# Kernel tuning notes

Measured on AMD Instinct MI355X. Metric: run time of the kernel, lower is better.

The kernel has to match this reference:

```python
import jax, jax.numpy as jnp
import numpy as np

D_MODEL = 1024
D_FF = 4096
N_EXPERTS = 4
D_HID = D_MODEL // 2
TOP_K = 2
B, T = 2, 4096


def setup_inputs() -> dict:
    key = jax.random.key(0)
    ks = jax.random.split(key, 10)
    s_in = 1.0 / np.sqrt(D_MODEL)
    s_ff = 1.0 / np.sqrt(D_FF)
    s_h = 1.0 / np.sqrt(D_HID)
    return {
        "x": jax.random.normal(ks[0], (B, T, D_MODEL), jnp.float32),
        # stacked expert FFN params [E, ...]
        "w1": jax.random.normal(ks[1], (N_EXPERTS, D_MODEL, D_FF), jnp.float32) * s_in,
        "b1": jnp.zeros((N_EXPERTS, D_FF), jnp.float32),
        "w2": jax.random.normal(ks[2], (N_EXPERTS, D_FF, D_MODEL), jnp.float32) * s_ff,
        "b2": jnp.zeros((N_EXPERTS, D_MODEL), jnp.float32),
        # router MLP params
        "wr1": jax.random.normal(ks[3], (D_MODEL, D_HID), jnp.float32) * s_in,
        "br1": jnp.zeros((D_HID,), jnp.float32),
        "wr2": jax.random.normal(ks[4], (D_HID, N_EXPERTS), jnp.float32) * s_h,
        "br2": jnp.zeros((N_EXPERTS,), jnp.float32),
    }


def _gelu(x):
    return jax.nn.gelu(x, approximate=False)  # torch nn.GELU default is exact erf


def reference(x, w1, b1, w2, b2, wr1, br1, wr2, br2):
    # Router: 2-layer MLP -> logits [B,T,E]
    h = _gelu(jnp.einsum('btd,dh->bth', x, wr1) + br1)
    logits = jnp.einsum('bth,he->bte', h, wr2) + br2
    # top-k masked softmax over experts
    top_vals, _ = jax.lax.top_k(logits, TOP_K)
    thresh = top_vals[..., -1:]
    masked = jnp.where(logits >= thresh, logits, -jnp.inf)
    gate = jax.nn.softmax(masked, axis=-1)  # [B,T,E], zeros off top-k
    # dense all-experts FFN: hid [B,T,E,d_ff]
    hid = _gelu(jnp.einsum('btd,edf->btef', x, w1) + b1)
    expert_outs = jnp.einsum('btef,efd->bted', hid, w2) + b2  # [B,T,E,d_model]
    out = jnp.einsum('bte,bted->btd', gate, expert_outs)
    return out, gate
```

## Files before the change

kernel.cpp:

```cpp
#include <hip/hip_runtime.h>

#define NTOK 8192
#define DM 1024
#define DF 4096
#define DH 512
#define NE 4
#define SLOTS (NTOK * 2)
#define NYT_MAX 132

typedef unsigned short ushort_t;
typedef short bf16x8 __attribute__((ext_vector_type(8)));
typedef float f32x4 __attribute__((ext_vector_type(4)));

__device__ __forceinline__ unsigned short f2bf(float f) {
    unsigned int u = __float_as_uint(f);
    u += 0x7FFFu + ((u >> 16) & 1u);
    return (unsigned short)(u >> 16);
}
__device__ __forceinline__ float bf2f(unsigned short h) {
    return __uint_as_float(((unsigned int)h) << 16);
}
__device__ __forceinline__ float gelu_exact(float x) {
    return 0.5f * x * (1.0f + erff(x * 0.7071067811865476f));
}
__device__ __forceinline__ float gelu_fast(float x) {
    float u = 1.5957691216057308f * (x + 0.044715f * x * x * x);
    return x / (1.0f + __expf(-u));
}
__device__ __forceinline__ void gload16(const void* g, void* l) {
    __builtin_amdgcn_global_load_lds((__attribute__((address_space(1))) void*)(g),
                                     (__attribute__((address_space(3))) void*)(l), 16, 0, 0);
}
__device__ __forceinline__ int swz(int b) { return b ^ (((b >> 7) & 3) << 4); }
__device__ __forceinline__ int imin(int a, int b) { return a < b ? a : b; }

#define WAIT_VM(N) asm volatile("s_waitcnt vmcnt(" #N ")" ::: "memory")
#define WAIT_LGKM0() asm volatile("s_waitcnt lgkmcnt(0)" ::: "memory")
#define SBAR() __builtin_amdgcn_s_barrier()
#define SCHED0() __builtin_amdgcn_sched_barrier(0)

__global__ __launch_bounds__(256) void k_cast_split(const float* __restrict__ in,
                                                    ushort_t* __restrict__ hi,
                                                    ushort_t* __restrict__ lo, int n4) {
    int i = blockIdx.x * 256 + threadIdx.x;
    if (i >= n4) return;
    float4 v = ((const float4*)in)[i];
    ushort4 h, l;
    h.x = f2bf(v.x); l.x = f2bf(v.x - bf2f(h.x));
    h.y = f2bf(v.y); l.y = f2bf(v.y - bf2f(h.y));
    h.z = f2bf(v.z); l.z = f2bf(v.z - bf2f(h.z));
    h.w = f2bf(v.w); l.w = f2bf(v.w - bf2f(h.w));
    ((ushort4*)hi)[i] = h;
    ((ushort4*)lo)[i] = l;
}

template <bool SPLIT>
__global__ __launch_bounds__(256) void k_tcast(const float* __restrict__ in,
                                               ushort_t* __restrict__ oh,
                                               ushort_t* __restrict__ ol, int K, int N) {
    __shared__ float t[64][65];
    size_t base = (size_t)blockIdx.z * K * N;
    const float* src = in + base;
    int k0 = blockIdx.y * 64, n0 = blockIdx.x * 64;
    int tx = threadIdx.x & 63, ty = threadIdx.x >> 6;
#pragma unroll
    for (int i = 0; i < 16; i++) {
        int r = ty + i * 4;
        t[r][tx] = src[(size_t)(k0 + r) * N + n0 + tx];
    }
    __syncthreads();
#pragma unroll
    for (int i = 0; i < 16; i++) {
        int nn = ty + i * 4;
        float v = t[tx][nn];
        unsigned short hv = f2bf(v);
        size_t o = base + (size_t)(n0 + nn) * K + k0 + tx;
        oh[o] = hv;
        if (SPLIT) ol[o] = f2bf(v - bf2f(hv));
    }
}

__global__ __launch_bounds__(256) void k_rgemm(
    const ushort_t* __restrict__ A0, const ushort_t* __restrict__ B0,
    const ushort_t* __restrict__ A1, const ushort_t* __restrict__ B1,
    const ushort_t* __restrict__ A2, const ushort_t* __restrict__ B2,
    int K, int N, const float* __restrict__ bias, float* __restrict__ outF)
{
    __shared__ ushort_t lA[3][4096];
    __shared__ ushort_t lB[3][4096];
    int row0 = blockIdx.y * 128, col0 = blockIdx.x * 128;
    int tid = threadIdx.x, lane = tid & 63, wv = tid >> 6;
    int wr = wv >> 1, wc = wv & 1;
    int r15 = lane & 15, hq = lane >> 4;

    f32x4 z = {0.f, 0.f, 0.f, 0.f};
    f32x4 acc[4][4];
#pragma unroll
    for (int m = 0; m < 4; m++)
#pragma unroll
        for (int n = 0; n < 4; n++) acc[m][n] = z;

    int d0 = tid * 16, d1 = d0 + 4096;
    int u0 = swz(d0), u1 = swz(d1);
    int rA0 = u0 >> 6, ko0 = ((u0 >> 4) & 3) * 8;
    int rA1 = u1 >> 6, ko1 = ((u1 >> 4) & 3) * 8;
    int nstep = K / 32;

#pragma unroll 1
    for (int p = 0; p < 3; p++) {
        const ushort_t* A = (p == 0) ? A0 : ((p == 1) ? A1 : A2);
        const ushort_t* B = (p == 0) ? B0 : ((p == 1) ? B1 : B2);
        const ushort_t* Ab0 = A + (size_t)(row0 + rA0) * K + ko0;
        const ushort_t* Ab1 = A + (size_t)(row0 + rA1) * K + ko1;
        const ushort_t* Bb0 = B + (size_t)(col0 + rA0) * K + ko0;
        const ushort_t* Bb1 = B + (size_t)(col0 + rA1) * K + ko1;

        auto stage = [&](int b, int s) {
            int kt = s * 32;
            char* la = (char*)lA + b * 8192;
            char* lb = (char*)lB + b * 8192;
            gload16(Ab0 + kt, la + wv * 1024);
            gload16(Ab1 + kt, la + 4096 + wv * 1024);
            gload16(Bb0 + kt, lb + wv * 1024);
            gload16(Bb1 + kt, lb + 4096 + wv * 1024);
        };
        auto compute = [&](int b) {
            const char* pa = (const char*)lA + b * 8192;
            const char* pb = (const char*)lB + b * 8192;
            bf16x8 af[4], bfr[4];
#pragma unroll
            for (int m = 0; m < 4; m++)
                af[m] = *(const bf16x8*)(pa + swz(((wr * 64 + m * 16 + r15) << 6) + (hq << 4)));
#pragma unroll
            for (int n = 0; n < 4; n++)
                bfr[n] = *(const bf16x8*)(pb + swz(((wc * 64 + n * 16 + r15) << 6) + (hq << 4)));
            __builtin_amdgcn_s_setprio(1);
#pragma unroll
            for (int m = 0; m < 4; m++)
#pragma unroll
                for (int n = 0; n < 4; n++)
                    acc[m][n] = __builtin_amdgcn_mfma_f32_16x16x32_bf16(af[m], bfr[n], acc[m][n], 0, 0, 0);
            __builtin_amdgcn_s_setprio(0);
        };

        stage(0, 0); stage(1, 1); stage(2, 2);
        int cur = 0;
#pragma unroll 1
        for (int s = 0; s < nstep - 3; s++) {
            WAIT_VM(8); SBAR(); SCHED0();
            compute(cur);
            WAIT_LGKM0(); SCHED0(); SBAR(); SCHED0();
            stage(cur, s + 3);
            cur = (cur == 2) ? 0 : cur + 1;
        }
        WAIT_VM(8); SBAR(); SCHED0();
        compute(cur); cur = (cur == 2) ? 0 : cur + 1;
        WAIT_VM(4); SBAR(); SCHED0();
        compute(cur); cur = (cur == 2) ? 0 : cur + 1;
        WAIT_VM(0); SBAR(); SCHED0();
        compute(cur);
        WAIT_LGKM0(); SCHED0(); SBAR(); SCHED0();
    }

#pragma unroll
    for (int m = 0; m < 4; m++)
#pragma unroll
        for (int q = 0; q < 4; q++) {
            int row = row0 + wr * 64 + m * 16 + hq * 4 + q;
#pragma unroll
            for (int n = 0; n < 4; n++) {
                int col = col0 + wc * 64 + n * 16 + r15;
                outF[(size_t)row * N + col] = gelu_exact(acc[m][n][q] + bias[col]);
            }
        }
}

template <int MODE>
__global__ __launch_bounds__(512, 4) void k_egemm(
    const ushort_t* __restrict__ A0, const ushort_t* __restrict__ B0,
    const float* __restrict__ bias, const float* __restrict__ gate,
    const int* __restrict__ idx, const int4* __restrict__ tiles,
    const int* __restrict__ meta,
    ushort_t* __restrict__ ghid, float* __restrict__ outA)
{
    constexpr int K = (MODE == 1) ? DM : DF;
    constexpr int NFULL = (MODE == 1) ? DF : DM;
    constexpr int NXT = NFULL / 256;
    constexpr int nwg = NXT * NYT_MAX;
    constexpr int q8 = nwg / 8;
    constexpr int NSTEP = K / 32;

    int bid = blockIdx.x;
    int wgid = (bid & 7) * q8 + (bid >> 3);
    int xt = wgid / NYT_MAX, yt = wgid % NYT_MAX;
    if (yt >= meta[0]) return;
    int4 ti = tiles[yt];
    int e = ti.x, rstart = ti.y, rows = ti.z, gbase = ti.w;
    int col0 = xt * 256;

    __shared__ ushort_t lA[3][4096];
    __shared__ ushort_t lB[3][8192];
    int tid = threadIdx.x, lane = tid & 63, wv = tid >> 6;
    int wr = wv >> 2, wc = wv & 3;
    int r15 = lane & 15, hq = lane >> 4;

    f32x4 z = {0.f, 0.f, 0.f, 0.f};
    f32x4 acc[4][4];
#pragma unroll
    for (int m = 0; m < 4; m++)
#pragma unroll
        for (int n = 0; n < 4; n++) acc[m][n] = z;

    int u = swz(tid * 16);
    int rA = u >> 6;
    int ko = ((u >> 4) & 3) * 8;
    const ushort_t *Ab, *Bb0, *Bb1;
    if (MODE == 1) {
        int tok = idx[e * NTOK + rstart + imin(rA, rows - 1)];
        Ab = A0 + (size_t)tok * K + ko;
    } else {
        Ab = A0 + (size_t)(gbase + imin(rA, rows - 1)) * K + ko;
    }
    Bb0 = B0 + ((size_t)e * NFULL + col0 + rA) * K + ko;
    Bb1 = B0 + ((size_t)e * NFULL + col0 + 128 + rA) * K + ko;

    auto stage = [&](int b, int s) {
        int kt = s * 32;
        gload16(Ab + kt, (char*)lA + b * 8192 + wv * 1024);
        gload16(Bb0 + kt, (char*)lB + b * 16384 + wv * 1024);
        gload16(Bb1 + kt, (char*)lB + b * 16384 + 8192 + wv * 1024);
    };
    auto compute = [&](int b) {
        const char* pa = (const char*)lA + b * 8192;
        const char* pb = (const char*)lB + b * 16384;
        bf16x8 af[4], bfr[4];
#pragma unroll
        for (int m = 0; m < 4; m++)
            af[m] = *(const bf16x8*)(pa + swz(((wr * 64 + m * 16 + r15) << 6) + (hq << 4)));
#pragma unroll
        for (int n = 0; n < 4; n++)
            bfr[n] = *(const bf16x8*)(pb + swz(((wc * 64 + n * 16 + r15) << 6) + (hq << 4)));
        __builtin_amdgcn_s_setprio(1);
#pragma unroll
        for (int m = 0; m < 4; m++)
#pragma unroll
            for (int n = 0; n < 4; n++)
                acc[m][n] = __builtin_amdgcn_mfma_f32_16x16x32_bf16(af[m], bfr[n], acc[m][n], 0, 0, 0);
        __builtin_amdgcn_s_setprio(0);
    };

    stage(0, 0); stage(1, 1); stage(2, 2);
    int cur = 0;
#pragma unroll 1
    for (int s = 0; s < NSTEP - 3; s++) {
        WAIT_VM(6); SBAR(); SCHED0();
        compute(cur);
        WAIT_LGKM0(); SCHED0(); SBAR(); SCHED0();
        stage(cur, s + 3);
        cur = (cur == 2) ? 0 : cur + 1;
    }
    WAIT_VM(6); SBAR(); SCHED0();
    compute(cur); cur = (cur == 2) ? 0 : cur + 1;
    WAIT_VM(3); SBAR(); SCHED0();
    compute(cur); cur = (cur == 2) ? 0 : cur + 1;
    WAIT_VM(0); SBAR(); SCHED0();
    compute(cur);

    if (MODE == 1) {
#pragma unroll
        for (int m = 0; m < 4; m++)
#pragma unroll
            for (int q = 0; q < 4; q++) {
                int lr = wr * 64 + m * 16 + hq * 4 + q;
                if (lr < rows) {
                    int token = idx[e * NTOK + rstart + lr];
                    float g = gate[token * 4 + e];
                    size_t rb = (size_t)(gbase + lr) * NFULL;
#pragma unroll
                    for (int n = 0; n < 4; n++) {
                        int col = col0 + wc * 64 + n * 16 + r15;
                        float v = gelu_fast(acc[m][n][q] + bias[(size_t)e * NFULL + col]) * g;
                        ghid[rb + col] = f2bf(v);
                    }
                }
            }
    } else {
#pragma unroll
        for (int m = 0; m < 4; m++)
#pragma unroll
            for (int q = 0; q < 4; q++) {
                int lr = wr * 64 + m * 16 + hq * 4 + q;
                if (lr < rows) {
                    int token = idx[e * NTOK + rstart + lr];
#pragma unroll
                    for (int n = 0; n < 4; n++) {
                        int col = col0 + wc * 64 + n * 16 + r15;
                        atomicAdd(&outA[(size_t)token * NFULL + col], acc[m][n][q]);
                    }
                }
            }
    }
}

__global__ __launch_bounds__(256) void k_gate(const float* __restrict__ h,
                                              const float* __restrict__ wr2,
                                              const float* __restrict__ br2,
                                              float* __restrict__ gate,
                                              int* __restrict__ cnt,
                                              int* __restrict__ idx) {
    int t = blockIdx.x * 4 + (threadIdx.x >> 6);
    int lane = threadIdx.x & 63;
    const float* hr = h + (size_t)t * DH;
    const float4* w4 = (const float4*)wr2;
    float gx = 0.f, gy = 0.f, gz = 0.f, gw = 0.f;
#pragma unroll
    for (int j = 0; j < 8; j++) {
        int k = lane * 8 + j;
        float hv = hr[k];
        float4 w = w4[k];
        gx += hv * w.x; gy += hv * w.y; gz += hv * w.z; gw += hv * w.w;
    }
#pragma unroll
    for (int off = 32; off > 0; off >>= 1) {
        gx += __shfl_xor(gx, off);
        gy += __shfl_xor(gy, off);
        gz += __shfl_xor(gz, off);
        gw += __shfl_xor(gw, off);
    }
    if (lane == 0) {
        float ls[4];
        ls[0] = gx + br2[0]; ls[1] = gy + br2[1]; ls[2] = gz + br2[2]; ls[3] = gw + br2[3];
        int i1 = 0; float m1 = ls[0];
#pragma unroll
        for (int i = 1; i < 4; i++) if (ls[i] > m1) { m1 = ls[i]; i1 = i; }
        int i2 = -1; float m2 = -1e30f;
#pragma unroll
        for (int i = 0; i < 4; i++) if (i != i1 && ls[i] > m2) { m2 = ls[i]; i2 = i; }
        float e0 = (ls[0] >= m2) ? expf(ls[0] - m1) : 0.f;
        float e1 = (ls[1] >= m2) ? expf(ls[1] - m1) : 0.f;
        float e2 = (ls[2] >= m2) ? expf(ls[2] - m1) : 0.f;
        float e3 = (ls[3] >= m2) ? expf(ls[3] - m1) : 0.f;
        float iz = 1.f / (e0 + e1 + e2 + e3);
        float4 g = {e0 * iz, e1 * iz, e2 * iz, e3 * iz};
        ((float4*)gate)[t] = g;
        int s0 = atomicAdd(&cnt[i1], 1);
        idx[i1 * NTOK + s0] = t;
        int s1 = atomicAdd(&cnt[i2], 1);
        idx[i2 * NTOK + s1] = t;
    }
}

__global__ void k_tiles(const int* __restrict__ cnt, int4* __restrict__ tiles,
                        int* __restrict__ meta) {
    if (threadIdx.x != 0 || blockIdx.x != 0) return;
    int base = 0, nt = 0;
    for (int e = 0; e < NE; e++) {
        int c = cnt[e];
        for (int r = 0; r < c; r += 128) {
            int4 ti;
            ti.x = e; ti.y = r; ti.z = (c - r < 128) ? (c - r) : 128; ti.w = base + r;
            tiles[nt++] = ti;
        }
        base += c;
    }
    meta[0] = nt;
}

__global__ __launch_bounds__(256) void k_init_out(const float* __restrict__ gate,
                                                  const float* __restrict__ b2,
                                                  float* __restrict__ out) {
    int i = blockIdx.x * 256 + threadIdx.x;
    int t = i >> 8;
    int c4 = i & 255;
    float4 g = ((const float4*)gate)[t];
    const float4* b = (const float4*)b2;
    float4 v0 = b[c4], v1 = b[256 + c4], v2 = b[512 + c4], v3 = b[768 + c4];
    float4 o;
    o.x = g.x * v0.x + g.y * v1.x + g.z * v2.x + g.w * v3.x;
    o.y = g.x * v0.y + g.y * v1.y + g.z * v2.y + g.w * v3.y;
    o.z = g.x * v0.z + g.y * v1.z + g.z * v2.z + g.w * v3.z;
    o.w = g.x * v0.w + g.y * v1.w + g.z * v2.w + g.w * v3.w;
    ((float4*)out)[i] = o;
}

extern "C" void kernel_launch(void* const* d_in, const int* in_sizes, int n_in,
                              void* d_out, int out_size, void* d_ws, size_t ws_size,
                              hipStream_t stream) {
    const float* x   = (const float*)d_in[0];
    const float* w1  = (const float*)d_in[1];
    const float* b1  = (const float*)d_in[2];
    const float* w2  = (const float*)d_in[3];
    const float* b2  = (const float*)d_in[4];
    const float* wr1 = (const float*)d_in[5];
    const float* br1 = (const float*)d_in[6];
    const float* wr2 = (const float*)d_in[7];
    const float* br2 = (const float*)d_in[8];
    float* out  = (float*)d_out;
    float* gate = out + (size_t)NTOK * DM;

    char* p = (char*)d_ws;
    auto take = [&](size_t bytes) { char* r = p; p += (bytes + 255) & ~(size_t)255; return r; };
    ushort_t* xh    = (ushort_t*)take((size_t)NTOK * DM * 2);
    ushort_t* w1T   = (ushort_t*)take((size_t)NE * DF * DM * 2);
    ushort_t* w2T   = (ushort_t*)take((size_t)NE * DM * DF * 2);
    ushort_t* wr1Th = (ushort_t*)take((size_t)DH * DM * 2);
    ushort_t* wr1Tl = (ushort_t*)take((size_t)DH * DM * 2);
    int*      cnt   = (int*)take(64);
    int*      idx   = (int*)take((size_t)NE * NTOK * 4);
    int4*     tiles = (int4*)take(144 * 16);
    int*      meta  = (int*)take(64);
    char*     region = take((size_t)SLOTS * DF * 2);
    ushort_t* xl    = (ushort_t*)region;
    float*    h     = (float*)(region + (size_t)NTOK * DM * 2);
    ushort_t* ghid  = (ushort_t*)region;

    hipMemsetAsync(cnt, 0, 64, stream);

    k_cast_split<<<NTOK * DM / 4 / 256, 256, 0, stream>>>(x, xh, xl, NTOK * DM / 4);
    k_tcast<false><<<dim3(DF / 64, DM / 64, NE), 256, 0, stream>>>(w1, w1T, nullptr, DM, DF);
    k_tcast<false><<<dim3(DM / 64, DF / 64, NE), 256, 0, stream>>>(w2, w2T, nullptr, DF, DM);
    k_tcast<true ><<<dim3(DH / 64, DM / 64, 1),  256, 0, stream>>>(wr1, wr1Th, wr1Tl, DM, DH);

    k_rgemm<<<dim3(DH / 128, NTOK / 128), 256, 0, stream>>>(
        xh, wr1Th, xh, wr1Tl, xl, wr1Th, DM, DH, br1, h);
    k_gate<<<NTOK / 4, 256, 0, stream>>>(h, wr2, br2, gate, cnt, idx);
    k_tiles<<<1, 64, 0, stream>>>(cnt, tiles, meta);
    k_init_out<<<NTOK * DM / 4 / 256, 256, 0, stream>>>(gate, b2, out);

    k_egemm<1><<<(DF / 256) * NYT_MAX, 512, 0, stream>>>(
        xh, w1T, b1, gate, idx, tiles, meta, ghid, nullptr);
    k_egemm<2><<<(DM / 256) * NYT_MAX, 512, 0, stream>>>(
        ghid, w2T, nullptr, gate, idx, tiles, meta, nullptr, out);
}
```

Before: 941.9 us.

## Split router GEMM passes across grid, widen expert tiles, split-K second expert GEMM

Router GEMM now runs its three split-precision passes as separate blocks along grid z and combines them with atomic adds into a zeroed buffer, with bias and GELU moved into the gate kernel. The gate kernel handles 64 tokens per block and does one batched atomic per expert per block instead of one per token. The expert GEMMs move to 256-thread blocks with 128x256 per-wave-pair tiles (4x8 MFMA accumulators), a new block-to-tile mapping for MODE 1, and a two-way split-K over DF for MODE 2. The aim is more parallelism and fewer atomics in routing, plus more reuse per block in the expert GEMMs. The cost is extra atomic traffic, higher register pressure, and a memset.

```diff
diff --git a/kernel.cpp b/kernel.cpp
--- a/kernel.cpp
+++ b/kernel.cpp
@@ -80,15 +80,19 @@
     }
 }
 
-__global__ __launch_bounds__(256) void k_rgemm(
+__global__ __launch_bounds__(256, 3) void k_rgemm(
     const ushort_t* __restrict__ A0, const ushort_t* __restrict__ B0,
     const ushort_t* __restrict__ A1, const ushort_t* __restrict__ B1,
     const ushort_t* __restrict__ A2, const ushort_t* __restrict__ B2,
-    int K, int N, const float* __restrict__ bias, float* __restrict__ outF)
+    float* __restrict__ hraw)
 {
+    constexpr int K = DM, N = DH;
     __shared__ ushort_t lA[3][4096];
     __shared__ ushort_t lB[3][4096];
     int row0 = blockIdx.y * 128, col0 = blockIdx.x * 128;
+    int p = blockIdx.z;
+    const ushort_t* A = (p == 0) ? A0 : ((p == 1) ? A1 : A2);
+    const ushort_t* B = (p == 0) ? B0 : ((p == 1) ? B1 : B2);
     int tid = threadIdx.x, lane = tid & 63, wv = tid >> 6;
     int wr = wv >> 1, wc = wv & 1;
     int r15 = lane & 15, hq = lane >> 4;
@@ -103,64 +107,56 @@
     int d0 = tid * 16, d1 = d0 + 4096;
     int u0 = swz(d0), u1 = swz(d1);
     int rA0 = u0 >> 6, ko0 = ((u0 >> 4) & 3) * 8;
-    int rA1 = u1 >> 6, ko1 = ((u1 >> 4) & 3) * 8;
-    int nstep = K / 32;
-
+    int rA1 = (u1 >> 6) & 63, ko1 = ((u1 >> 4) & 3) * 8;
+    const ushort_t* Ab0 = A + (size_t)(row0 + rA0) * K + ko0;
+    const ushort_t* Ab1 = A + (size_t)(row0 + 64 + rA1) * K + ko1;
+    const ushort_t* Bb0 = B + (size_t)(col0 + rA0) * K + ko0;
+    const ushort_t* Bb1 = B + (size_t)(col0 + 64 + rA1) * K + ko1;
+
+    auto stage = [&](int b, int s) {
+        int kt = s * 32;
+        char* la = (char*)lA + b * 8192;
+        char* lb = (char*)lB + b * 8192;
+        gload16(Ab0 + kt, la + wv * 1024);
+        gload16(Ab1 + kt, la + 4096 + wv * 1024);
+        gload16(Bb0 + kt, lb + wv * 1024);
+        gload16(Bb1 + kt, lb + 4096 + wv * 1024);
+    };
+    auto compute = [&](int b) {
+        const char* pa = (const char*)lA + b * 8192;
+        const char* pb = (const char*)lB + b * 8192;
+        bf16x8 af[4], bfr[4];
+#pragma unroll
+        for (int m = 0; m < 4; m++)
+            af[m] = *(const bf16x8*)(pa + swz(((wr * 64 + m * 16 + r15) << 6) + (hq << 4)));
+#pragma unroll
+        for (int n = 0; n < 4; n++)
+            bfr[n] = *(const bf16x8*)(pb + swz(((wc * 64 + n * 16 + r15) << 6) + (hq << 4)));
+        __builtin_amdgcn_s_setprio(1);
+#pragma unroll
+        for (int m = 0; m < 4; m++)
+#pragma unroll
+            for (int n = 0; n < 4; n++)
+                acc[m][n] = __builtin_amdgcn_mfma_f32_16x16x32_bf16(af[m], bfr[n], acc[m][n], 0, 0, 0);
+        __builtin_amdgcn_s_setprio(0);
+    };
+
+    stage(0, 0); stage(1, 1); stage(2, 2);
+    int cur = 0;
 #pragma unroll 1
-    for (int p = 0; p < 3; p++) {
-        const ushort_t* A = (p == 0) ? A0 : ((p == 1) ? A1 : A2);
-        const ushort_t* B = (p == 0) ? B0 : ((p == 1) ? B1 : B2);
-        const ushort_t* Ab0 = A + (size_t)(row0 + rA0) * K + ko0;
-        const ushort_t* Ab1 = A + (size_t)(row0 + rA1) * K + ko1;
-        const ushort_t* Bb0 = B + (size_t)(col0 + rA0) * K + ko0;
-        const ushort_t* Bb1 = B + (size_t)(col0 + rA1) * K + ko1;
-
-        auto stage = [&](int b, int s) {
-            int kt = s * 32;
-            char* la = (char*)lA + b * 8192;
-            char* lb = (char*)lB + b * 8192;
-            gload16(Ab0 + kt, la + wv * 1024);
-            gload16(Ab1 + kt, la + 4096 + wv * 1024);
-            gload16(Bb0 + kt, lb + wv * 1024);
-            gload16(Bb1 + kt, lb + 4096 + wv * 1024);
-        };
-        auto compute = [&](int b) {
-            const char* pa = (const char*)lA + b * 8192;
-            const char* pb = (const char*)lB + b * 8192;
-            bf16x8 af[4], bfr[4];
-#pragma unroll
-            for (int m = 0; m < 4; m++)
-                af[m] = *(const bf16x8*)(pa + swz(((wr * 64 + m * 16 + r15) << 6) + (hq << 4)));
-#pragma unroll
-            for (int n = 0; n < 4; n++)
-                bfr[n] = *(const bf16x8*)(pb + swz(((wc * 64 + n * 16 + r15) << 6) + (hq << 4)));
-            __builtin_amdgcn_s_setprio(1);
-#pragma unroll
-            for (int m = 0; m < 4; m++)
-#pragma unroll
-                for (int n = 0; n < 4; n++)
-                    acc[m][n] = __builtin_amdgcn_mfma_f32_16x16x32_bf16(af[m], bfr[n], acc[m][n], 0, 0, 0);
-            __builtin_amdgcn_s_setprio(0);
-        };
-
-        stage(0, 0); stage(1, 1); stage(2, 2);
-        int cur = 0;
-#pragma unroll 1
-        for (int s = 0; s < nstep - 3; s++) {
-            WAIT_VM(8); SBAR(); SCHED0();
-            compute(cur);
-            WAIT_LGKM0(); SCHED0(); SBAR(); SCHED0();
-            stage(cur, s + 3);
-            cur = (cur == 2) ? 0 : cur + 1;
-        }
+    for (int s = 0; s < K / 32 - 3; s++) {
         WAIT_VM(8); SBAR(); SCHED0();
-        compute(cur); cur = (cur == 2) ? 0 : cur + 1;
-        WAIT_VM(4); SBAR(); SCHED0();
-        compute(cur); cur = (cur == 2) ? 0 : cur + 1;
-        WAIT_VM(0); SBAR(); SCHED0();
         compute(cur);
         WAIT_LGKM0(); SCHED0(); SBAR(); SCHED0();
-    }
+        stage(cur, s + 3);
+        cur = (cur == 2) ? 0 : cur + 1;
+    }
+    WAIT_VM(8); SBAR(); SCHED0();
+    compute(cur); cur = (cur == 2) ? 0 : cur + 1;
+    WAIT_VM(4); SBAR(); SCHED0();
+    compute(cur); cur = (cur == 2) ? 0 : cur + 1;
+    WAIT_VM(0); SBAR(); SCHED0();
+    compute(cur);
 
 #pragma unroll
     for (int m = 0; m < 4; m++)
@@ -170,29 +166,35 @@
 #pragma unroll
             for (int n = 0; n < 4; n++) {
                 int col = col0 + wc * 64 + n * 16 + r15;
-                outF[(size_t)row * N + col] = gelu_exact(acc[m][n][q] + bias[col]);
+                atomicAdd(&hraw[(size_t)row * N + col], acc[m][n][q]);
             }
         }
 }
 
 template <int MODE>
-__global__ __launch_bounds__(512, 4) void k_egemm(
+__global__ __launch_bounds__(256, 2) void k_egemm(
     const ushort_t* __restrict__ A0, const ushort_t* __restrict__ B0,
     const float* __restrict__ bias, const float* __restrict__ gate,
     const int* __restrict__ idx, const int4* __restrict__ tiles,
     const int* __restrict__ meta,
     ushort_t* __restrict__ ghid, float* __restrict__ outA)
 {
-    constexpr int K = (MODE == 1) ? DM : DF;
+    constexpr int KF = (MODE == 1) ? DM : DF;
     constexpr int NFULL = (MODE == 1) ? DF : DM;
-    constexpr int NXT = NFULL / 256;
-    constexpr int nwg = NXT * NYT_MAX;
-    constexpr int q8 = nwg / 8;
-    constexpr int NSTEP = K / 32;
+    constexpr int NS = (MODE == 1) ? (DM / 32) : (2048 / 32);
 
     int bid = blockIdx.x;
-    int wgid = (bid & 7) * q8 + (bid >> 3);
-    int xt = wgid / NYT_MAX, yt = wgid % NYT_MAX;
+    int xt, yt, kbase = 0;
+    if (MODE == 1) {
+        int wgid = (bid & 7) * 264 + (bid >> 3);
+        if (wgid < 2048) { int s = wgid >> 7; int r = wgid & 127; xt = r >> 3; yt = s * 8 + (r & 7); }
+        else             { int r = wgid - 2048;  xt = r >> 2;     yt = 128 + (r & 3); }
+    } else {
+        int pair = bid & 7;
+        yt = bid >> 3;
+        kbase = (pair >> 2) * 2048;
+        xt = pair & 3;
+    }
     if (yt >= meta[0]) return;
     int4 ti = tiles[yt];
     int e = ti.x, rstart = ti.y, rows = ti.z, gbase = ti.w;
@@ -201,50 +203,70 @@
     __shared__ ushort_t lA[3][4096];
     __shared__ ushort_t lB[3][8192];
     int tid = threadIdx.x, lane = tid & 63, wv = tid >> 6;
-    int wr = wv >> 2, wc = wv & 3;
+    int wr = wv >> 1, wc = wv & 1;
     int r15 = lane & 15, hq = lane >> 4;
 
     f32x4 z = {0.f, 0.f, 0.f, 0.f};
-    f32x4 acc[4][4];
+    f32x4 acc[4][8];
 #pragma unroll
     for (int m = 0; m < 4; m++)
 #pragma unroll
-        for (int n = 0; n < 4; n++) acc[m][n] = z;
-
-    int u = swz(tid * 16);
-    int rA = u >> 6;
-    int ko = ((u >> 4) & 3) * 8;
-    const ushort_t *Ab, *Bb0, *Bb1;
+        for (int n = 0; n < 8; n++) acc[m][n] = z;
+
+    int uA0 = swz(tid * 16);
+    int uA1 = swz(tid * 16 + 4096);
+    int uB0 = swz(tid * 16);
+    int uB1 = swz(tid * 16 + 4096);
+    int uB2 = swz(tid * 16 + 8192);
+    int uB3 = swz(tid * 16 + 12288);
+    int rA0 = uA0 >> 6, kA0 = ((uA0 >> 4) & 3) * 8;
+    int rA1 = uA1 >> 6, kA1 = ((uA1 >> 4) & 3) * 8;
+    int rB0 = uB0 >> 6, kB0 = ((uB0 >> 4) & 3) * 8;
+    int rB1 = uB1 >> 6, kB1 = ((uB1 >> 4) & 3) * 8;
+    int rB2 = uB2 >> 6, kB2 = ((uB2 >> 4) & 3) * 8;
+    int rB3 = uB3 >> 6, kB3 = ((uB3 >> 4) & 3) * 8;
+
+    const ushort_t *Ab0, *Ab1;
     if (MODE == 1) {
-        int tok = idx[e * NTOK + rstart + imin(rA, rows - 1)];
-        Ab = A0 + (size_t)tok * K + ko;
+        int t0 = idx[e * NTOK + rstart + imin(rA0, rows - 1)];
+        int t1 = idx[e * NTOK + rstart + imin(rA1, rows - 1)];
+        Ab0 = A0 + (size_t)t0 * KF + kA0;
+        Ab1 = A0 + (size_t)t1 * KF + kA1;
     } else {
-        Ab = A0 + (size_t)(gbase + imin(rA, rows - 1)) * K + ko;
-    }
-    Bb0 = B0 + ((size_t)e * NFULL + col0 + rA) * K + ko;
-    Bb1 = B0 + ((size_t)e * NFULL + col0 + 128 + rA) * K + ko;
+        Ab0 = A0 + (size_t)(gbase + imin(rA0, rows - 1)) * KF + kbase + kA0;
+        Ab1 = A0 + (size_t)(gbase + imin(rA1, rows - 1)) * KF + kbase + kA1;
+    }
+    const ushort_t* Bb0 = B0 + ((size_t)e * NFULL + col0 + rB0) * KF + kbase + kB0;
+    const ushort_t* Bb1 = B0 + ((size_t)e * NFULL + col0 + rB1) * KF + kbase + kB1;
+    const ushort_t* Bb2 = B0 + ((size_t)e * NFULL + col0 + rB2) * KF + kbase + kB2;
+    const ushort_t* Bb3 = B0 + ((size_t)e * NFULL + col0 + rB3) * KF + kbase + kB3;
 
     auto stage = [&](int b, int s) {
         int kt = s * 32;
-        gload16(Ab + kt, (char*)lA + b * 8192 + wv * 1024);
-        gload16(Bb0 + kt, (char*)lB + b * 16384 + wv * 1024);
-        gload16(Bb1 + kt, (char*)lB + b * 16384 + 8192 + wv * 1024);
+        char* la = (char*)lA + b * 8192;
+        char* lb = (char*)lB + b * 16384;
+        gload16(Ab0 + kt, la + wv * 1024);
+        gload16(Ab1 + kt, la + 4096 + wv * 1024);
+        gload16(Bb0 + kt, lb + wv * 1024);
+        gload16(Bb1 + kt, lb + 4096 + wv * 1024);
+        gload16(Bb2 + kt, lb + 8192 + wv * 1024);
+        gload16(Bb3 + kt, lb + 12288 + wv * 1024);
     };
     auto compute = [&](int b) {
         const char* pa = (const char*)lA + b * 8192;
         const char* pb = (const char*)lB + b * 16384;
-        bf16x8 af[4], bfr[4];
+        bf16x8 af[4], bfr[8];
 #pragma unroll
         for (int m = 0; m < 4; m++)
             af[m] = *(const bf16x8*)(pa + swz(((wr * 64 + m * 16 + r15) << 6) + (hq << 4)));
 #pragma unroll
-        for (int n = 0; n < 4; n++)
-            bfr[n] = *(const bf16x8*)(pb + swz(((wc * 64 + n * 16 + r15) << 6) + (hq << 4)));
+        for (int n = 0; n < 8; n++)
+            bfr[n] = *(const bf16x8*)(pb + swz(((wc * 128 + n * 16 + r15) << 6) + (hq << 4)));
         __builtin_amdgcn_s_setprio(1);
 #pragma unroll
         for (int m = 0; m < 4; m++)
 #pragma unroll
-            for (int n = 0; n < 4; n++)
+            for (int n = 0; n < 8; n++)
                 acc[m][n] = __builtin_amdgcn_mfma_f32_16x16x32_bf16(af[m], bfr[n], acc[m][n], 0, 0, 0);
         __builtin_amdgcn_s_setprio(0);
     };
@@ -252,16 +274,16 @@
     stage(0, 0); stage(1, 1); stage(2, 2);
     int cur = 0;
 #pragma unroll 1
-    for (int s = 0; s < NSTEP - 3; s++) {
-        WAIT_VM(6); SBAR(); SCHED0();
+    for (int s = 0; s < NS - 3; s++) {
+        WAIT_VM(12); SBAR(); SCHED0();
         compute(cur);
         WAIT_LGKM0(); SCHED0(); SBAR(); SCHED0();
         stage(cur, s + 3);
         cur = (cur == 2) ? 0 : cur + 1;
     }
+    WAIT_VM(12); SBAR(); SCHED0();
+    compute(cur); cur = (cur == 2) ? 0 : cur + 1;
     WAIT_VM(6); SBAR(); SCHED0();
-    compute(cur); cur = (cur == 2) ? 0 : cur + 1;
-    WAIT_VM(3); SBAR(); SCHED0();
     compute(cur); cur = (cur == 2) ? 0 : cur + 1;
     WAIT_VM(0); SBAR(); SCHED0();
     compute(cur);
@@ -277,8 +299,8 @@
                     float g = gate[token * 4 + e];
                     size_t rb = (size_t)(gbase + lr) * NFULL;
 #pragma unroll
-                    for (int n = 0; n < 4; n++) {
-                        int col = col0 + wc * 64 + n * 16 + r15;
+                    for (int n = 0; n < 8; n++) {
+                        int col = col0 + wc * 128 + n * 16 + r15;
                         float v = gelu_fast(acc[m][n][q] + bias[(size_t)e * NFULL + col]) * g;
                         ghid[rb + col] = f2bf(v);
                     }
@@ -293,8 +315,8 @@
                 if (lr < rows) {
                     int token = idx[e * NTOK + rstart + lr];
 #pragma unroll
-                    for (int n = 0; n < 4; n++) {
-                        int col = col0 + wc * 64 + n * 16 + r15;
+                    for (int n = 0; n < 8; n++) {
+                        int col = col0 + wc * 128 + n * 16 + r15;
                         atomicAdd(&outA[(size_t)token * NFULL + col], acc[m][n][q]);
                     }
                 }
@@ -302,32 +324,39 @@
     }
 }
 
-__global__ __launch_bounds__(256) void k_gate(const float* __restrict__ h,
+__global__ __launch_bounds__(256) void k_gate(const float* __restrict__ hraw,
+                                              const float* __restrict__ br1,
                                               const float* __restrict__ wr2,
                                               const float* __restrict__ br2,
                                               float* __restrict__ gate,
                                               int* __restrict__ cnt,
-                                              int* __restrict__ idx) {
-    int t = blockIdx.x * 4 + (threadIdx.x >> 6);
-    int lane = threadIdx.x & 63;
-    const float* hr = h + (size_t)t * DH;
+                                              int* __restrict__ idxo) {
+    __shared__ int smE[128];
+    int tid = threadIdx.x;
+    int tl = tid >> 2, q = tid & 3;
+    int token = blockIdx.x * 64 + tl;
+    const float4* h4 = (const float4*)(hraw + (size_t)token * DH + q * 128);
+    const float4* b4 = (const float4*)(br1 + q * 128);
     const float4* w4 = (const float4*)wr2;
     float gx = 0.f, gy = 0.f, gz = 0.f, gw = 0.f;
 #pragma unroll
-    for (int j = 0; j < 8; j++) {
-        int k = lane * 8 + j;
-        float hv = hr[k];
-        float4 w = w4[k];
-        gx += hv * w.x; gy += hv * w.y; gz += hv * w.z; gw += hv * w.w;
-    }
-#pragma unroll
-    for (int off = 32; off > 0; off >>= 1) {
-        gx += __shfl_xor(gx, off);
-        gy += __shfl_xor(gy, off);
-        gz += __shfl_xor(gz, off);
-        gw += __shfl_xor(gw, off);
-    }
-    if (lane == 0) {
+    for (int j = 0; j < 32; j++) {
+        float4 hv = h4[j];
+        float4 bb = b4[j];
+        float h0 = gelu_exact(hv.x + bb.x), h1 = gelu_exact(hv.y + bb.y);
+        float h2 = gelu_exact(hv.z + bb.z), h3 = gelu_exact(hv.w + bb.w);
+        int k = q * 128 + j * 4;
+        float4 w0 = w4[k], w1 = w4[k + 1], w2v = w4[k + 2], w3 = w4[k + 3];
+        gx += h0 * w0.x + h1 * w1.x + h2 * w2v.x + h3 * w3.x;
+        gy += h0 * w0.y + h1 * w1.y + h2 * w2v.y + h3 * w3.y;
+        gz += h0 * w0.z + h1 * w1.z + h2 * w2v.z + h3 * w3.z;
+        gw += h0 * w0.w + h1 * w1.w + h2 * w2v.w + h3 * w3.w;
+    }
+    gx += __shfl_xor(gx, 1); gx += __shfl_xor(gx, 2);
+    gy += __shfl_xor(gy, 1); gy += __shfl_xor(gy, 2);
+    gz += __shfl_xor(gz, 1); gz += __shfl_xor(gz, 2);
+    gw += __shfl_xor(gw, 1); gw += __shfl_xor(gw, 2);
+    if (q == 0) {
         float ls[4];
         ls[0] = gx + br2[0]; ls[1] = gy + br2[1]; ls[2] = gz + br2[2]; ls[3] = gw + br2[3];
         int i1 = 0; float m1 = ls[0];
@@ -342,11 +371,18 @@
         float e3 = (ls[3] >= m2) ? expf(ls[3] - m1) : 0.f;
         float iz = 1.f / (e0 + e1 + e2 + e3);
         float4 g = {e0 * iz, e1 * iz, e2 * iz, e3 * iz};
-        ((float4*)gate)[t] = g;
-        int s0 = atomicAdd(&cnt[i1], 1);
-        idx[i1 * NTOK + s0] = t;
-        int s1 = atomicAdd(&cnt[i2], 1);
-        idx[i2 * NTOK + s1] = t;
+        ((float4*)gate)[token] = g;
+        smE[tl * 2] = i1;
+        smE[tl * 2 + 1] = i2;
+    }
+    __syncthreads();
+    if (tid < NE) {
+        int e = tid, c = 0;
+        for (int s = 0; s < 128; s++) c += (smE[s] == e);
+        int base = atomicAdd(&cnt[e], c);
+        int r = 0;
+        for (int s = 0; s < 128; s++)
+            if (smE[s] == e) idxo[e * NTOK + base + (r++)] = blockIdx.x * 64 + (s >> 1);
     }
 }
 
@@ -415,20 +451,21 @@
     ushort_t* ghid  = (ushort_t*)region;
 
     hipMemsetAsync(cnt, 0, 64, stream);
+    hipMemsetAsync(h, 0, (size_t)NTOK * DH * 4, stream);
 
     k_cast_split<<<NTOK * DM / 4 / 256, 256, 0, stream>>>(x, xh, xl, NTOK * DM / 4);
     k_tcast<false><<<dim3(DF / 64, DM / 64, NE), 256, 0, stream>>>(w1, w1T, nullptr, DM, DF);
     k_tcast<false><<<dim3(DM / 64, DF / 64, NE), 256, 0, stream>>>(w2, w2T, nullptr, DF, DM);
     k_tcast<true ><<<dim3(DH / 64, DM / 64, 1),  256, 0, stream>>>(wr1, wr1Th, wr1Tl, DM, DH);
 
-    k_rgemm<<<dim3(DH / 128, NTOK / 128), 256, 0, stream>>>(
-        xh, wr1Th, xh, wr1Tl, xl, wr1Th, DM, DH, br1, h);
-    k_gate<<<NTOK / 4, 256, 0, stream>>>(h, wr2, br2, gate, cnt, idx);
+    k_rgemm<<<dim3(DH / 128, NTOK / 128, 3), 256, 0, stream>>>(
+        xh, wr1Th, xh, wr1Tl, xl, wr1Th, h);
+    k_gate<<<NTOK / 64, 256, 0, stream>>>(h, br1, wr2, br2, gate, cnt, idx);
     k_tiles<<<1, 64, 0, stream>>>(cnt, tiles, meta);
     k_init_out<<<NTOK * DM / 4 / 256, 256, 0, stream>>>(gate, b2, out);
 
-    k_egemm<1><<<(DF / 256) * NYT_MAX, 512, 0, stream>>>(
+    k_egemm<1><<<16 * NYT_MAX, 256, 0, stream>>>(
         xh, w1T, b1, gate, idx, tiles, meta, ghid, nullptr);
-    k_egemm<2><<<(DM / 256) * NYT_MAX, 512, 0, stream>>>(
+    k_egemm<2><<<8 * NYT_MAX, 256, 0, stream>>>(
         ghid, w2T, nullptr, gate, idx, tiles, meta, nullptr, out);
 }
```

After: 880.8 us. 1.07x faster.
